# Optimization experiments

Hardware: AMD Instinct MI355X
Metric: run time of the kernel (lower is better)

The kernel has to match this reference:

```python
import jax, jax.numpy as jnp
import numpy as np

N = 16384
D_IN = 512
HEADS = 2
D_HEAD = 256
EPS_LN = 1e-5
NEG_SLOPE = 0.2


def l2norm_dim0(x):
    # F.normalize(x, p=2, dim=0): per-column L2 normalization
    n = jnp.sqrt(jnp.sum(x * x, axis=0, keepdims=True))
    return x / jnp.maximum(n, 1e-12)


def layer_norm(x, g, b):
    m = jnp.mean(x, axis=-1, keepdims=True)
    v = jnp.mean((x - m) ** 2, axis=-1, keepdims=True)
    return (x - m) * jax.lax.rsqrt(v + EPS_LN) * g + b


def gat_conv(x, edge_index, W, att_src, att_dst, bias):
    # PyG GATConv with add_self_loops=True, concat=True, negative_slope=0.2
    n = x.shape[0]
    loops = jnp.arange(n, dtype=edge_index.dtype)
    src = jnp.concatenate([edge_index[0], loops])
    dst = jnp.concatenate([edge_index[1], loops])
    h = (x @ W).reshape(n, HEADS, D_HEAD)            # [N, H, Dh]
    a_src = jnp.sum(h * att_src, axis=-1)            # [N, H]
    a_dst = jnp.sum(h * att_dst, axis=-1)            # [N, H]
    e = a_src[src] + a_dst[dst]                      # [E, H]
    e = jnp.where(e >= 0, e, NEG_SLOPE * e)          # leaky_relu
    # segment softmax over incoming edges of each dst node
    emax = jax.ops.segment_max(e, dst, num_segments=n)
    ex = jnp.exp(e - emax[dst])
    den = jax.ops.segment_sum(ex, dst, num_segments=n)
    alpha = ex / den[dst]                            # [E, H]
    msg = h[src] * alpha[:, :, None]                 # [E, H, Dh]
    out = jax.ops.segment_sum(msg, dst, num_segments=n)  # [N, H, Dh]
    return out.reshape(n, HEADS * D_HEAD) + bias


def setup_inputs() -> dict:
    key = jax.random.key(0)
    ks = jax.random.split(key, 16)
    def glorot(k, shape):
        lim = np.sqrt(6.0 / (shape[0] + shape[-1]))
        return jax.random.uniform(k, shape, jnp.float32, -lim, lim)
    x = jax.random.normal(ks[0], (N, D_IN), jnp.float32)
    edge_index = jax.random.randint(ks[1], (2, 524288), 0, N, jnp.int64)
    return {
        "x": x,
        "edge_index": edge_index,
        "W": glorot(ks[2], (D_IN, HEADS * D_HEAD)),
        "att_src": glorot(ks[3], (HEADS, D_HEAD)),
        "att_dst": glorot(ks[4], (HEADS, D_HEAD)),
        "bias_conv": jnp.zeros((HEADS * D_HEAD,), jnp.float32),
        "Wa": glorot(ks[5], (512, 256)), "ba": jnp.zeros((256,), jnp.float32),
        "ga": jnp.ones((256,), jnp.float32), "bga": jnp.zeros((256,), jnp.float32),
        "W1": glorot(ks[6], (256, 128)), "b1": jnp.zeros((128,), jnp.float32),
        "g1": jnp.ones((128,), jnp.float32), "bg1": jnp.zeros((128,), jnp.float32),
        "W2": glorot(ks[7], (128, 64)), "b2": jnp.zeros((64,), jnp.float32),
        "g2": jnp.ones((64,), jnp.float32), "bg2": jnp.zeros((64,), jnp.float32),
        "W3": glorot(ks[8], (64, 3)), "b3": jnp.zeros((3,), jnp.float32),
    }


def reference(x, edge_index, W, att_src, att_dst, bias_conv,
              Wa, ba, ga, bga, W1, b1, g1, bg1,
              W2, b2, g2, bg2, W3, b3):
    h = l2norm_dim0(x)
    h = gat_conv(h, edge_index, W, att_src, att_dst, bias_conv)
    h = jax.nn.relu(h)
    h = l2norm_dim0(h)
    h = layer_norm(h @ Wa + ba, ga, bga)
    h = jax.nn.relu(h)
    h = l2norm_dim0(h)
    h = layer_norm(h @ W1 + b1, g1, bg1)
    h = jax.nn.relu(h)
    h = l2norm_dim0(h)
    h = layer_norm(h @ W2 + b2, g2, bg2)
    h = jax.nn.relu(h)
    h = l2norm_dim0(h)
    h = h @ W3 + b3                                  # [N, 3]
    # torch.cdist(h, h, p=2)
    sq = jnp.sum(h * h, axis=-1)
    d2 = sq[:, None] + sq[None, :] - 2.0 * (h @ h.T)
    return jnp.sqrt(jnp.maximum(d2, 0.0))
```

## Files before the change

### kernel.cpp

```cpp
#include <hip/hip_runtime.h>
#include <math.h>


typedef __bf16 bf16x8 __attribute__((ext_vector_type(8)));
typedef __bf16 bf16x4 __attribute__((ext_vector_type(4)));
typedef __bf16 bf16x2 __attribute__((ext_vector_type(2)));
typedef float  f32x4  __attribute__((ext_vector_type(4)));
typedef short  short8 __attribute__((ext_vector_type(8)));

static __device__ __forceinline__ float leaky02(float e){ return e >= 0.f ? e : 0.2f*e; }

static __device__ __forceinline__ float wred_sum(float v){
  #pragma unroll
  for (int m = 1; m < 64; m <<= 1) v += __shfl_xor(v, m);
  return v;
}
static __device__ __forceinline__ float wred_max(float v){
  #pragma unroll
  for (int m = 1; m < 64; m <<= 1) v = fmaxf(v, __shfl_xor(v, m));
  return v;
}

__global__ void colnorm_sq(const float* __restrict__ X, float* __restrict__ ss, int R, int C){
  int c = blockIdx.x*blockDim.x + threadIdx.x;
  if (c >= C) return;
  int r0 = blockIdx.y * 128;
  int r1 = r0 + 128; if (r1 > R) r1 = R;
  float s = 0.f;
  for (int r = r0; r < r1; ++r){ float v = X[(size_t)r*C + c]; s = fmaf(v, v, s); }
  atomicAdd(&ss[c], s);
}

__global__ void scale_rows(const float* __restrict__ W, const float* __restrict__ ss,
                           float* __restrict__ Wo, int K, int C){
  int i = blockIdx.x*blockDim.x + threadIdx.x;
  if (i >= K*C) return;
  int row = i / C;
  float n = fmaxf(sqrtf(ss[row]), 1e-12f);
  Wo[i] = W[i] / n;
}

__global__ __launch_bounds__(256) void split_hl(const float* __restrict__ X,
    __bf16* __restrict__ H, __bf16* __restrict__ L, int n4){
  int i = blockIdx.x*256 + threadIdx.x;
  if (i >= n4) return;
  float4 v = ((const float4*)X)[i];
  bf16x4 hv, lv;
  hv[0] = (__bf16)v.x; lv[0] = (__bf16)(v.x - (float)hv[0]);
  hv[1] = (__bf16)v.y; lv[1] = (__bf16)(v.y - (float)hv[1]);
  hv[2] = (__bf16)v.z; lv[2] = (__bf16)(v.z - (float)hv[2]);
  hv[3] = (__bf16)v.w; lv[3] = (__bf16)(v.w - (float)hv[3]);
  ((bf16x4*)H)[i] = hv;
  ((bf16x4*)L)[i] = lv;
}

__global__ __launch_bounds__(256) void split_tr_scaled(const float* __restrict__ B,
    const float* __restrict__ ss,
    __bf16* __restrict__ TH, __bf16* __restrict__ TL, int K, int N){
  __shared__ float tile[32][33];
  int lx = threadIdx.x & 31, ly = threadIdx.x >> 5;
  int kb = blockIdx.y*32, nb = blockIdx.x*32;
  #pragma unroll
  for (int i = 0; i < 4; i++){
    int kr = kb + ly + i*8;
    float inv = 1.f / fmaxf(sqrtf(ss[kr]), 1e-12f);
    tile[ly + i*8][lx] = B[(size_t)kr*N + nb + lx] * inv;
  }
  __syncthreads();
  #pragma unroll
  for (int i = 0; i < 4; i++){
    int nl = ly + i*8;
    float v = tile[lx][nl];
    __bf16 h = (__bf16)v;
    TH[(size_t)(nb + nl)*K + kb + lx] = h;
    TL[(size_t)(nb + nl)*K + kb + lx] = (__bf16)(v - (float)h);
  }
}

__global__ __launch_bounds__(256) void gemm_bf16x3(
    const __bf16* __restrict__ Ah, const __bf16* __restrict__ Al,
    const __bf16* __restrict__ Bth, const __bf16* __restrict__ Btl,
    float* __restrict__ C, int M, int N, int K)
{
  __shared__ __align__(16) __bf16 sAh[128][40];
  __shared__ __align__(16) __bf16 sAl[128][40];
  __shared__ __align__(16) __bf16 sBh[64][40];
  __shared__ __align__(16) __bf16 sBl[64][40];
  int tid = threadIdx.x;
  int lane = tid & 63, wave = tid >> 6;
  int wr = wave >> 1, wc = wave & 1;
  int rowBase = blockIdx.x << 7, colBase = blockIdx.y << 6;

  int ar = tid >> 2;
  int ac = tid & 3;

  short8 rAh0, rAh1, rAl0, rAl1, rBh, rBl;
  auto loadA = [&](int k0){
    rAh0 = *(const short8*)(Ah + (size_t)(rowBase + ar     )*K + k0 + ac*8);
    rAh1 = *(const short8*)(Ah + (size_t)(rowBase + ar + 64)*K + k0 + ac*8);
    rAl0 = *(const short8*)(Al + (size_t)(rowBase + ar     )*K + k0 + ac*8);
    rAl1 = *(const short8*)(Al + (size_t)(rowBase + ar + 64)*K + k0 + ac*8);
    rBh  = *(const short8*)(Bth + (size_t)(colBase + ar)*K + k0 + ac*8);
    rBl  = *(const short8*)(Btl + (size_t)(colBase + ar)*K + k0 + ac*8);
  };

  f32x4 acc[4][2];
  #pragma unroll
  for (int m = 0; m < 4; m++)
    #pragma unroll
    for (int n = 0; n < 2; n++) acc[m][n] = (f32x4){0.f,0.f,0.f,0.f};

  loadA(0);
  int nsteps = K >> 5;
  for (int s = 0; s < nsteps; ++s){
    __syncthreads();
    *(short8*)&sAh[ar][ac*8]      = rAh0;
    *(short8*)&sAh[ar+64][ac*8]   = rAh1;
    *(short8*)&sAl[ar][ac*8]      = rAl0;
    *(short8*)&sAl[ar+64][ac*8]   = rAl1;
    *(short8*)&sBh[ar][ac*8]      = rBh;
    *(short8*)&sBl[ar][ac*8]      = rBl;
    if (s + 1 < nsteps) loadA((s+1) << 5);
    __syncthreads();

    int kslot = lane >> 4;
    bf16x8 fah[4], fal[4], fbh[2], fbl[2];
    #pragma unroll
    for (int m = 0; m < 4; m++){
      int r = wr*64 + m*16 + (lane & 15);
      fah[m] = *(const bf16x8*)&sAh[r][kslot*8];
      fal[m] = *(const bf16x8*)&sAl[r][kslot*8];
    }
    #pragma unroll
    for (int n = 0; n < 2; n++){
      int c = wc*32 + n*16 + (lane & 15);
      fbh[n] = *(const bf16x8*)&sBh[c][kslot*8];
      fbl[n] = *(const bf16x8*)&sBl[c][kslot*8];
    }
    #pragma unroll
    for (int m = 0; m < 4; m++)
      #pragma unroll
      for (int n = 0; n < 2; n++){
        acc[m][n] = __builtin_amdgcn_mfma_f32_16x16x32_bf16(fah[m], fbh[n], acc[m][n], 0,0,0);
        acc[m][n] = __builtin_amdgcn_mfma_f32_16x16x32_bf16(fah[m], fbl[n], acc[m][n], 0,0,0);
        acc[m][n] = __builtin_amdgcn_mfma_f32_16x16x32_bf16(fal[m], fbh[n], acc[m][n], 0,0,0);
      }
  }

  int rg = lane >> 4, cl = lane & 15;
  #pragma unroll
  for (int m = 0; m < 4; m++)
    #pragma unroll
    for (int n = 0; n < 2; n++)
      #pragma unroll
      for (int j = 0; j < 4; j++)
        C[(size_t)(rowBase + wr*64 + m*16 + rg*4 + j)*N + colBase + wc*32 + n*16 + cl] = acc[m][n][j];
}

__global__ __launch_bounds__(256) void att_kernel(const float* __restrict__ h,
    const float* __restrict__ att_src, const float* __restrict__ att_dst,
    float* __restrict__ asrc, float* __restrict__ adst, int N){
  int lane = threadIdx.x & 63;
  int node = blockIdx.x*4 + (threadIdx.x >> 6);
  const float4* hp = (const float4*)(h + (size_t)node*512);
  float4 v0 = hp[lane], v1 = hp[64 + lane];
  float4 as0 = ((const float4*)att_src)[lane], as1 = ((const float4*)att_src)[64+lane];
  float4 ad0 = ((const float4*)att_dst)[lane], ad1 = ((const float4*)att_dst)[64+lane];
  float s0 = v0.x*as0.x + v0.y*as0.y + v0.z*as0.z + v0.w*as0.w;
  float s1 = v1.x*as1.x + v1.y*as1.y + v1.z*as1.z + v1.w*as1.w;
  float d0 = v0.x*ad0.x + v0.y*ad0.y + v0.z*ad0.z + v0.w*ad0.w;
  float d1 = v1.x*ad1.x + v1.y*ad1.y + v1.z*ad1.z + v1.w*ad1.w;
  s0 = wred_sum(s0); s1 = wred_sum(s1); d0 = wred_sum(d0); d1 = wred_sum(d1);
  if (lane == 0){
    asrc[2*node] = s0; asrc[2*node+1] = s1;
    adst[2*node] = d0; adst[2*node+1] = d1;
  }
}

__global__ void deg_count(const int* __restrict__ dst, int* deg, int E){
  int e = blockIdx.x*blockDim.x + threadIdx.x;
  if (e < E) atomicAdd(&deg[dst[e]], 1);
}
__global__ __launch_bounds__(1024) void scan_kernel(const int* __restrict__ deg,
    int* __restrict__ offs, int* __restrict__ cursor, int n){
  __shared__ int part[1024];
  int t = threadIdx.x;
  int chunk = (n + 1023) >> 10;
  int base = t * chunk;
  int loc[32];
  int local = 0;
  for (int k = 0; k < chunk; k++){
    int idx = base + k; loc[k] = local;
    if (idx < n) local += deg[idx] + 1;
  }
  part[t] = local; __syncthreads();
  for (int off = 1; off < 1024; off <<= 1){
    int v = (t >= off) ? part[t-off] : 0; __syncthreads();
    part[t] += v; __syncthreads();
  }
  int excl = part[t] - local;
  for (int k = 0; k < chunk; k++){
    int idx = base + k;
    if (idx < n){ int o = excl + loc[k]; offs[idx] = o; cursor[idx] = o; }
  }
  if (t == 1023) offs[n] = part[1023];
}
__global__ void scatter_edges(const int* __restrict__ src, const int* __restrict__ dst,
                              int* cursor, int* __restrict__ ssrc, int E, int N){
  int e = blockIdx.x*blockDim.x + threadIdx.x;
  if (e < E){
    int d = dst[e]; int pos = atomicAdd(&cursor[d], 1); ssrc[pos] = src[e];
  } else if (e < E + N){
    int i = e - E; int pos = atomicAdd(&cursor[i], 1); ssrc[pos] = i;
  }
}

__global__ __launch_bounds__(256) void gat_aggregate(const float* __restrict__ h,
    const int* __restrict__ offs, const int* __restrict__ ssrc,
    const float* __restrict__ asrc, const float* __restrict__ adst,
    const float* __restrict__ bias, float* __restrict__ out,
    __bf16* __restrict__ H, __bf16* __restrict__ L, int N){
  __shared__ float cw[2][4];
  __shared__ int sidx[256];
  __shared__ float salpha[512];
  int d = blockIdx.x, t = threadIdx.x, lane = t & 63, wid = t >> 6;
  int beg = offs[d], end = offs[d+1], cnt = end - beg;
  float ad0 = adst[2*d], ad1 = adst[2*d+1];
  int dim = 2*t, head = t >> 7;
  float accx = 0.f, accy = 0.f;

  if (cnt <= 256){
    float le0 = -1e30f, le1 = -1e30f;
    if (t < cnt){
      int s = ssrc[beg + t]; sidx[t] = s;
      float2 a = *(const float2*)&asrc[2*s];
      le0 = leaky02(a.x + ad0); le1 = leaky02(a.y + ad1);
    }
    float m0 = wred_max(le0), m1 = wred_max(le1);
    if (lane == 0){ cw[0][wid] = m0; cw[1][wid] = m1; }
    __syncthreads();
    m0 = fmaxf(fmaxf(cw[0][0],cw[0][1]), fmaxf(cw[0][2],cw[0][3]));
    m1 = fmaxf(fmaxf(cw[1][0],cw[1][1]), fmaxf(cw[1][2],cw[1][3]));
    __syncthreads();
    float e0 = (t < cnt) ? __expf(le0 - m0) : 0.f;
    float e1 = (t < cnt) ? __expf(le1 - m1) : 0.f;
    float q0 = wred_sum(e0), q1 = wred_sum(e1);
    if (lane == 0){ cw[0][wid] = q0; cw[1][wid] = q1; }
    __syncthreads();
    float inv0 = 1.f / (cw[0][0]+cw[0][1]+cw[0][2]+cw[0][3]);
    float inv1 = 1.f / (cw[1][0]+cw[1][1]+cw[1][2]+cw[1][3]);
    if (t < cnt){ salpha[2*t] = e0*inv0; salpha[2*t+1] = e1*inv1; }
    __syncthreads();
    #pragma unroll 2
    for (int o = 0; o < cnt; ++o){
      int s = sidx[o];
      float al = salpha[2*o + head];
      float2 v = *(const float2*)&h[(size_t)s*512 + dim];
      accx = fmaf(al, v.x, accx); accy = fmaf(al, v.y, accy);
    }
  } else {
    float m0 = -1e30f, m1 = -1e30f;
    for (int o = beg + t; o < end; o += 256){
      int s = ssrc[o]; float2 a = *(const float2*)&asrc[2*s];
      m0 = fmaxf(m0, leaky02(a.x + ad0)); m1 = fmaxf(m1, leaky02(a.y + ad1));
    }
    m0 = wred_max(m0); m1 = wred_max(m1);
    if (lane == 0){ cw[0][wid] = m0; cw[1][wid] = m1; }
    __syncthreads();
    m0 = fmaxf(fmaxf(cw[0][0],cw[0][1]), fmaxf(cw[0][2],cw[0][3]));
    m1 = fmaxf(fmaxf(cw[1][0],cw[1][1]), fmaxf(cw[1][2],cw[1][3]));
    __syncthreads();
    float q0 = 0.f, q1 = 0.f;
    for (int o = beg + t; o < end; o += 256){
      int s = ssrc[o]; float2 a = *(const float2*)&asrc[2*s];
      q0 += __expf(leaky02(a.x + ad0) - m0); q1 += __expf(leaky02(a.y + ad1) - m1);
    }
    q0 = wred_sum(q0); q1 = wred_sum(q1);
    if (lane == 0){ cw[0][wid] = q0; cw[1][wid] = q1; }
    __syncthreads();
    float inv0 = 1.f / (cw[0][0]+cw[0][1]+cw[0][2]+cw[0][3]);
    float inv1 = 1.f / (cw[1][0]+cw[1][1]+cw[1][2]+cw[1][3]);
    __syncthreads();
    for (int c0 = beg; c0 < end; c0 += 256){
      int cc = end - c0; if (cc > 256) cc = 256;
      if (t < cc){
        int s = ssrc[c0 + t]; sidx[t] = s;
        float2 a = *(const float2*)&asrc[2*s];
        salpha[2*t]   = __expf(leaky02(a.x + ad0) - m0) * inv0;
        salpha[2*t+1] = __expf(leaky02(a.y + ad1) - m1) * inv1;
      }
      __syncthreads();
      for (int o = 0; o < cc; ++o){
        int s = sidx[o];
        float al = salpha[2*o + head];
        float2 v = *(const float2*)&h[(size_t)s*512 + dim];
        accx = fmaf(al, v.x, accx); accy = fmaf(al, v.y, accy);
      }
      __syncthreads();
    }
  }
  float ox = fmaxf(accx + bias[dim],   0.f);
  float oy = fmaxf(accy + bias[dim+1], 0.f);
  *(float2*)&out[(size_t)d*512 + dim] = make_float2(ox, oy);
  bf16x2 hv, lv;
  hv[0] = (__bf16)ox; lv[0] = (__bf16)(ox - (float)hv[0]);
  hv[1] = (__bf16)oy; lv[1] = (__bf16)(oy - (float)hv[1]);
  *(bf16x2*)&H[(size_t)d*512 + dim] = hv;
  *(bf16x2*)&L[(size_t)d*512 + dim] = lv;
}

template<int C, bool SPLIT>
__global__ __launch_bounds__(256) void ln_relu_t(float* __restrict__ Z,
    const float* __restrict__ bias, const float* __restrict__ g,
    const float* __restrict__ bg, __bf16* __restrict__ H, __bf16* __restrict__ L, int R){
  constexpr int VW = C / 64;
  int lane = threadIdx.x & 63, wid = threadIdx.x >> 6;
  int r = blockIdx.x*4 + wid;
  size_t base = (size_t)r*C + lane*VW;
  float v[VW], bi[VW], gm[VW], bt[VW];
  if constexpr (VW == 4){
    float4 t0 = *(const float4*)&Z[base];
    float4 t1 = *(const float4*)&bias[lane*4];
    float4 t2 = *(const float4*)&g[lane*4];
    float4 t3 = *(const float4*)&bg[lane*4];
    v[0]=t0.x; v[1]=t0.y; v[2]=t0.z; v[3]=t0.w;
    bi[0]=t1.x; bi[1]=t1.y; bi[2]=t1.z; bi[3]=t1.w;
    gm[0]=t2.x; gm[1]=t2.y; gm[2]=t2.z; gm[3]=t2.w;
    bt[0]=t3.x; bt[1]=t3.y; bt[2]=t3.z; bt[3]=t3.w;
  } else if constexpr (VW == 2){
    float2 t0 = *(const float2*)&Z[base];
    float2 t1 = *(const float2*)&bias[lane*2];
    float2 t2 = *(const float2*)&g[lane*2];
    float2 t3 = *(const float2*)&bg[lane*2];
    v[0]=t0.x; v[1]=t0.y; bi[0]=t1.x; bi[1]=t1.y;
    gm[0]=t2.x; gm[1]=t2.y; bt[0]=t3.x; bt[1]=t3.y;
  } else {
    v[0] = Z[base]; bi[0] = bias[lane]; gm[0] = g[lane]; bt[0] = bg[lane];
  }
  float sum = 0.f;
  #pragma unroll
  for (int j = 0; j < VW; j++){ v[j] += bi[j]; sum += v[j]; }
  sum = wred_sum(sum);
  float mean = sum * (1.f/C);
  float sq = 0.f;
  #pragma unroll
  for (int j = 0; j < VW; j++){ float dz = v[j]-mean; sq += dz*dz; }
  sq = wred_sum(sq);
  float rs = 1.f / sqrtf(sq*(1.f/C) + 1e-5f);
  float o[VW];
  #pragma unroll
  for (int j = 0; j < VW; j++) o[j] = fmaxf((v[j]-mean)*rs*gm[j] + bt[j], 0.f);
  if constexpr (VW == 4) *(float4*)&Z[base] = make_float4(o[0],o[1],o[2],o[3]);
  else if constexpr (VW == 2) *(float2*)&Z[base] = make_float2(o[0],o[1]);
  else Z[base] = o[0];
  if constexpr (SPLIT){
    if constexpr (VW == 4){
      bf16x4 hv, lv;
      #pragma unroll
      for (int j = 0; j < 4; j++){ hv[j] = (__bf16)o[j]; lv[j] = (__bf16)(o[j]-(float)hv[j]); }
      *(bf16x4*)&H[base] = hv; *(bf16x4*)&L[base] = lv;
    } else if constexpr (VW == 2){
      bf16x2 hv, lv;
      #pragma unroll
      for (int j = 0; j < 2; j++){ hv[j] = (__bf16)o[j]; lv[j] = (__bf16)(o[j]-(float)hv[j]); }
      *(bf16x2*)&H[base] = hv; *(bf16x2*)&L[base] = lv;
    } else {
      __bf16 hv = (__bf16)o[0];
      H[base] = hv; L[base] = (__bf16)(o[0]-(float)hv);
    }
  }
}

__global__ __launch_bounds__(256) void final_hf4(const float* __restrict__ A,
    const float* __restrict__ W3s, const float* __restrict__ b3,
    float4* __restrict__ hf4, int N){
  __shared__ float w[64*3];
  __shared__ float b[3];
  if (threadIdx.x < 192) w[threadIdx.x] = W3s[threadIdx.x];
  if (threadIdx.x < 3)   b[threadIdx.x] = b3[threadIdx.x];
  __syncthreads();
  int r = blockIdx.x*blockDim.x + threadIdx.x;
  if (r >= N) return;
  float x = b[0], y = b[1], z = b[2];
  #pragma unroll 8
  for (int k = 0; k < 64; ++k){
    float a = A[(size_t)r*64 + k];
    x = fmaf(a, w[k*3],   x);
    y = fmaf(a, w[k*3+1], y);
    z = fmaf(a, w[k*3+2], z);
  }
  float sq = x*x + y*y + z*z;
  hf4[r] = make_float4(x, y, z, sq);
}

__global__ __launch_bounds__(256) void cdist_kernel(const float4* __restrict__ hf,
                                                    float* __restrict__ out, int N){
  int i = blockIdx.y;
  int j0 = (blockIdx.x*256 + threadIdx.x)*4;
  float4 a = hf[i];
  float4 b0 = hf[j0], b1 = hf[j0+1], b2 = hf[j0+2], b3 = hf[j0+3];
  f32x4 r; float d;
  d = a.w + b0.w - 2.f*(a.x*b0.x + a.y*b0.y + a.z*b0.z); r[0] = sqrtf(fmaxf(d, 0.f));
  d = a.w + b1.w - 2.f*(a.x*b1.x + a.y*b1.y + a.z*b1.z); r[1] = sqrtf(fmaxf(d, 0.f));
  d = a.w + b2.w - 2.f*(a.x*b2.x + a.y*b2.y + a.z*b2.z); r[2] = sqrtf(fmaxf(d, 0.f));
  d = a.w + b3.w - 2.f*(a.x*b3.x + a.y*b3.y + a.z*b3.z); r[3] = sqrtf(fmaxf(d, 0.f));
  __builtin_nontemporal_store(r, (f32x4*)&out[(size_t)i*N + j0]);
}

extern "C" void kernel_launch(void* const* d_in, const int* in_sizes, int n_in,
                              void* d_out, int out_size, void* d_ws, size_t ws_size,
                              hipStream_t stream){
  const int N = in_sizes[0] / 512;
  const int E = in_sizes[1] / 2;

  const float* x         = (const float*)d_in[0];
  const int*   ei        = (const int*)  d_in[1];
  const float* W         = (const float*)d_in[2];
  const float* att_src   = (const float*)d_in[3];
  const float* att_dst   = (const float*)d_in[4];
  const float* bias_conv = (const float*)d_in[5];
  const float* Wa  = (const float*)d_in[6];
  const float* ba  = (const float*)d_in[7];
  const float* ga  = (const float*)d_in[8];
  const float* bga = (const float*)d_in[9];
  const float* W1  = (const float*)d_in[10];
  const float* b1  = (const float*)d_in[11];
  const float* g1  = (const float*)d_in[12];
  const float* bg1 = (const float*)d_in[13];
  const float* W2  = (const float*)d_in[14];
  const float* b2  = (const float*)d_in[15];
  const float* g2  = (const float*)d_in[16];
  const float* bg2 = (const float*)d_in[17];
  const float* W3  = (const float*)d_in[18];
  const float* b3  = (const float*)d_in[19];

  const int* e_src = ei;
  const int* e_dst = ei + E;

  size_t off = 0;
  auto alloc = [&](size_t bytes)->char*{
    size_t o = off; off += (bytes + 255) & ~(size_t)255;
    return (char*)d_ws + o;
  };
  float* bufA  = (float*)alloc((size_t)N*512*4);
  float* bufB  = (float*)alloc((size_t)N*512*4);
  __bf16* Ah   = (__bf16*)alloc((size_t)N*512*2);
  __bf16* Al   = (__bf16*)alloc((size_t)N*512*2);
  __bf16* Bth  = (__bf16*)alloc(512*512*2);
  __bf16* Btl  = (__bf16*)alloc(512*512*2);
  float* W3sc  = (float*)alloc(64*3*4);
  char* zbase  = alloc(5*512*4 + (size_t)N*4);
  float* ss1 = (float*)zbase;
  float* ss2 = ss1 + 512;
  float* ss3 = ss2 + 512;
  float* ss4 = ss3 + 512;
  float* ss5 = ss4 + 512;
  int*   deg = (int*)(ss5 + 512);
  float* asrc  = (float*)alloc((size_t)N*2*4);
  float* adst  = (float*)alloc((size_t)N*2*4);
  float4* hf4  = (float4*)alloc((size_t)N*16);
  int* offs    = (int*)alloc((size_t)(N+1)*4);
  int* cursor  = (int*)alloc((size_t)N*4);
  int* ssrc    = (int*)alloc((size_t)(E+N)*4);

  float* outF = (float*)d_out;

  hipMemsetAsync(zbase, 0, 5*512*4 + (size_t)N*4, stream);

  colnorm_sq<<<dim3(2,128), 256, 0, stream>>>(x, ss1, N, 512);
  split_hl<<<(N*512/4+255)/256, 256, 0, stream>>>(x, Ah, Al, N*512/4);
  split_tr_scaled<<<dim3(16,16), 256, 0, stream>>>(W, ss1, Bth, Btl, 512, 512);
  gemm_bf16x3<<<dim3(N/128, 8), 256, 0, stream>>>(Ah, Al, Bth, Btl, bufA, N, 512, 512);

  att_kernel<<<N/4, 256, 0, stream>>>(bufA, att_src, att_dst, asrc, adst, N);
  deg_count<<<(E+255)/256, 256, 0, stream>>>(e_dst, deg, E);
  scan_kernel<<<1, 1024, 0, stream>>>(deg, offs, cursor, N);
  scatter_edges<<<(E+N+255)/256, 256, 0, stream>>>(e_src, e_dst, cursor, ssrc, E, N);
  gat_aggregate<<<N, 256, 0, stream>>>(bufA, offs, ssrc, asrc, adst, bias_conv,
                                       bufB, Ah, Al, N);

  colnorm_sq<<<dim3(2,128), 256, 0, stream>>>(bufB, ss2, N, 512);
  split_tr_scaled<<<dim3(8,16), 256, 0, stream>>>(Wa, ss2, Bth, Btl, 512, 256);
  gemm_bf16x3<<<dim3(N/128, 4), 256, 0, stream>>>(Ah, Al, Bth, Btl, bufA, N, 256, 512);
  ln_relu_t<256,true><<<N/4, 256, 0, stream>>>(bufA, ba, ga, bga, Ah, Al, N);

  colnorm_sq<<<dim3(1,128), 256, 0, stream>>>(bufA, ss3, N, 256);
  split_tr_scaled<<<dim3(4,8), 256, 0, stream>>>(W1, ss3, Bth, Btl, 256, 128);
  gemm_bf16x3<<<dim3(N/128, 2), 256, 0, stream>>>(Ah, Al, Bth, Btl, bufB, N, 128, 256);
  ln_relu_t<128,true><<<N/4, 256, 0, stream>>>(bufB, b1, g1, bg1, Ah, Al, N);

  colnorm_sq<<<dim3(1,128), 256, 0, stream>>>(bufB, ss4, N, 128);
  split_tr_scaled<<<dim3(2,4), 256, 0, stream>>>(W2, ss4, Bth, Btl, 128, 64);
  gemm_bf16x3<<<dim3(N/128, 1), 256, 0, stream>>>(Ah, Al, Bth, Btl, bufA, N, 64, 128);
  ln_relu_t<64,false><<<N/4, 256, 0, stream>>>(bufA, b2, g2, bg2, (__bf16*)nullptr, (__bf16*)nullptr, N);

  colnorm_sq<<<dim3(1,128), 256, 0, stream>>>(bufA, ss5, N, 64);
  scale_rows<<<1, 256, 0, stream>>>(W3, ss5, W3sc, 64, 3);
  final_hf4<<<(N+255)/256, 256, 0, stream>>>(bufA, W3sc, b3, hf4, N);
  cdist_kernel<<<dim3(N/1024, N), 256, 0, stream>>>(hf4, outF, N);
}
```

Measured before the change: 765.1 us.

## Fuse input split into GEMM, wave-per-node GAT aggregation, drop fp32 GAT output

The first GEMM now reads fp32 x directly and splits it into bf16 hi/lo while staging to shared memory, which removes the separate split_hl pass over the input. GAT aggregation moves from one 256-thread block per node to one wave per node. Indices and attention weights are passed by shuffles instead of shared memory and barriers, and each lane loads 8 floats per neighbour. The fp32 GAT output write is removed, and its column norms are computed from the hi+lo bf16 pair. The W3 scaling is folded into final_hf4. The risk is more latency per wave on high-degree nodes and slightly different rounding in the norm.

Result: no change. 761.7 us (-0.4%).

```diff
diff --git a/kernel.cpp b/kernel.cpp
--- a/kernel.cpp
+++ b/kernel.cpp
@@ -31,27 +31,18 @@
   atomicAdd(&ss[c], s);
 }
 
-__global__ void scale_rows(const float* __restrict__ W, const float* __restrict__ ss,
-                           float* __restrict__ Wo, int K, int C){
-  int i = blockIdx.x*blockDim.x + threadIdx.x;
-  if (i >= K*C) return;
-  int row = i / C;
-  float n = fmaxf(sqrtf(ss[row]), 1e-12f);
-  Wo[i] = W[i] / n;
-}
-
-__global__ __launch_bounds__(256) void split_hl(const float* __restrict__ X,
-    __bf16* __restrict__ H, __bf16* __restrict__ L, int n4){
-  int i = blockIdx.x*256 + threadIdx.x;
-  if (i >= n4) return;
-  float4 v = ((const float4*)X)[i];
-  bf16x4 hv, lv;
-  hv[0] = (__bf16)v.x; lv[0] = (__bf16)(v.x - (float)hv[0]);
-  hv[1] = (__bf16)v.y; lv[1] = (__bf16)(v.y - (float)hv[1]);
-  hv[2] = (__bf16)v.z; lv[2] = (__bf16)(v.z - (float)hv[2]);
-  hv[3] = (__bf16)v.w; lv[3] = (__bf16)(v.w - (float)hv[3]);
-  ((bf16x4*)H)[i] = hv;
-  ((bf16x4*)L)[i] = lv;
+__global__ void colnorm_sq_hl(const __bf16* __restrict__ H, const __bf16* __restrict__ L,
+                              float* __restrict__ ss, int R, int C){
+  int c = blockIdx.x*blockDim.x + threadIdx.x;
+  if (c >= C) return;
+  int r0 = blockIdx.y * 128;
+  int r1 = r0 + 128; if (r1 > R) r1 = R;
+  float s = 0.f;
+  for (int r = r0; r < r1; ++r){
+    float v = (float)H[(size_t)r*C + c] + (float)L[(size_t)r*C + c];
+    s = fmaf(v, v, s);
+  }
+  atomicAdd(&ss[c], s);
 }
 
 __global__ __launch_bounds__(256) void split_tr_scaled(const float* __restrict__ B,
@@ -120,6 +111,93 @@
     *(short8*)&sAl[ar+64][ac*8]   = rAl1;
     *(short8*)&sBh[ar][ac*8]      = rBh;
     *(short8*)&sBl[ar][ac*8]      = rBl;
+    if (s + 1 < nsteps) loadA((s+1) << 5);
+    __syncthreads();
+
+    int kslot = lane >> 4;
+    bf16x8 fah[4], fal[4], fbh[2], fbl[2];
+    #pragma unroll
+    for (int m = 0; m < 4; m++){
+      int r = wr*64 + m*16 + (lane & 15);
+      fah[m] = *(const bf16x8*)&sAh[r][kslot*8];
+      fal[m] = *(const bf16x8*)&sAl[r][kslot*8];
+    }
+    #pragma unroll
+    for (int n = 0; n < 2; n++){
+      int c = wc*32 + n*16 + (lane & 15);
+      fbh[n] = *(const bf16x8*)&sBh[c][kslot*8];
+      fbl[n] = *(const bf16x8*)&sBl[c][kslot*8];
+    }
+    #pragma unroll
+    for (int m = 0; m < 4; m++)
+      #pragma unroll
+      for (int n = 0; n < 2; n++){
+        acc[m][n] = __builtin_amdgcn_mfma_f32_16x16x32_bf16(fah[m], fbh[n], acc[m][n], 0,0,0);
+        acc[m][n] = __builtin_amdgcn_mfma_f32_16x16x32_bf16(fah[m], fbl[n], acc[m][n], 0,0,0);
+        acc[m][n] = __builtin_amdgcn_mfma_f32_16x16x32_bf16(fal[m], fbh[n], acc[m][n], 0,0,0);
+      }
+  }
+
+  int rg = lane >> 4, cl = lane & 15;
+  #pragma unroll
+  for (int m = 0; m < 4; m++)
+    #pragma unroll
+    for (int n = 0; n < 2; n++)
+      #pragma unroll
+      for (int j = 0; j < 4; j++)
+        C[(size_t)(rowBase + wr*64 + m*16 + rg*4 + j)*N + colBase + wc*32 + n*16 + cl] = acc[m][n][j];
+}
+
+__global__ __launch_bounds__(256) void gemm_f32a_bf16x3(
+    const float* __restrict__ A,
+    const __bf16* __restrict__ Bth, const __bf16* __restrict__ Btl,
+    float* __restrict__ C, int M, int N, int K)
+{
+  __shared__ __align__(16) __bf16 sAh[128][40];
+  __shared__ __align__(16) __bf16 sAl[128][40];
+  __shared__ __align__(16) __bf16 sBh[64][40];
+  __shared__ __align__(16) __bf16 sBl[64][40];
+  int tid = threadIdx.x;
+  int lane = tid & 63, wave = tid >> 6;
+  int wr = wave >> 1, wc = wave & 1;
+  int rowBase = blockIdx.x << 7, colBase = blockIdx.y << 6;
+
+  int ar = tid >> 2;
+  int ac = tid & 3;
+
+  float4 rA0a, rA0b, rA1a, rA1b; short8 rBh, rBl;
+  auto loadA = [&](int k0){
+    const float* p0 = A + (size_t)(rowBase + ar)*K + k0 + ac*8;
+    rA0a = *(const float4*)p0; rA0b = *(const float4*)(p0 + 4);
+    const float* p1 = A + (size_t)(rowBase + ar + 64)*K + k0 + ac*8;
+    rA1a = *(const float4*)p1; rA1b = *(const float4*)(p1 + 4);
+    rBh  = *(const short8*)(Bth + (size_t)(colBase + ar)*K + k0 + ac*8);
+    rBl  = *(const short8*)(Btl + (size_t)(colBase + ar)*K + k0 + ac*8);
+  };
+  auto splitst = [&](float4 a, float4 b, __bf16* dh, __bf16* dl){
+    float t[8] = {a.x,a.y,a.z,a.w,b.x,b.y,b.z,b.w};
+    bf16x8 hv, lv;
+    #pragma unroll
+    for (int j = 0; j < 8; j++){
+      __bf16 h = (__bf16)t[j]; hv[j] = h; lv[j] = (__bf16)(t[j] - (float)h);
+    }
+    *(bf16x8*)dh = hv; *(bf16x8*)dl = lv;
+  };
+
+  f32x4 acc[4][2];
+  #pragma unroll
+  for (int m = 0; m < 4; m++)
+    #pragma unroll
+    for (int n = 0; n < 2; n++) acc[m][n] = (f32x4){0.f,0.f,0.f,0.f};
+
+  loadA(0);
+  int nsteps = K >> 5;
+  for (int s = 0; s < nsteps; ++s){
+    __syncthreads();
+    splitst(rA0a, rA0b, &sAh[ar][ac*8],    &sAl[ar][ac*8]);
+    splitst(rA1a, rA1b, &sAh[ar+64][ac*8], &sAl[ar+64][ac*8]);
+    *(short8*)&sBh[ar][ac*8] = rBh;
+    *(short8*)&sBl[ar][ac*8] = rBl;
     if (s + 1 < nsteps) loadA((s+1) << 5);
     __syncthreads();
 
@@ -215,98 +293,93 @@
   }
 }
 
-__global__ __launch_bounds__(256) void gat_aggregate(const float* __restrict__ h,
+__global__ __launch_bounds__(256) void gat_aggregate_w(const float* __restrict__ h,
     const int* __restrict__ offs, const int* __restrict__ ssrc,
     const float* __restrict__ asrc, const float* __restrict__ adst,
-    const float* __restrict__ bias, float* __restrict__ out,
+    const float* __restrict__ bias,
     __bf16* __restrict__ H, __bf16* __restrict__ L, int N){
-  __shared__ float cw[2][4];
-  __shared__ int sidx[256];
-  __shared__ float salpha[512];
-  int d = blockIdx.x, t = threadIdx.x, lane = t & 63, wid = t >> 6;
+  int lane = threadIdx.x & 63;
+  int d = blockIdx.x*4 + (threadIdx.x >> 6);
   int beg = offs[d], end = offs[d+1], cnt = end - beg;
   float ad0 = adst[2*d], ad1 = adst[2*d+1];
-  int dim = 2*t, head = t >> 7;
-  float accx = 0.f, accy = 0.f;
-
-  if (cnt <= 256){
-    float le0 = -1e30f, le1 = -1e30f;
-    if (t < cnt){
-      int s = ssrc[beg + t]; sidx[t] = s;
-      float2 a = *(const float2*)&asrc[2*s];
+
+  int dbase = lane*8;
+  bool head0 = dbase < 256;
+  f32x4 acc0 = {0.f,0.f,0.f,0.f}, acc1 = {0.f,0.f,0.f,0.f};
+
+  if (cnt <= 64){
+    int sreg = 0; float le0 = -1e30f, le1 = -1e30f;
+    if (lane < cnt){
+      sreg = ssrc[beg + lane];
+      float2 a = *(const float2*)&asrc[2*sreg];
       le0 = leaky02(a.x + ad0); le1 = leaky02(a.y + ad1);
     }
     float m0 = wred_max(le0), m1 = wred_max(le1);
-    if (lane == 0){ cw[0][wid] = m0; cw[1][wid] = m1; }
-    __syncthreads();
-    m0 = fmaxf(fmaxf(cw[0][0],cw[0][1]), fmaxf(cw[0][2],cw[0][3]));
-    m1 = fmaxf(fmaxf(cw[1][0],cw[1][1]), fmaxf(cw[1][2],cw[1][3]));
-    __syncthreads();
-    float e0 = (t < cnt) ? __expf(le0 - m0) : 0.f;
-    float e1 = (t < cnt) ? __expf(le1 - m1) : 0.f;
-    float q0 = wred_sum(e0), q1 = wred_sum(e1);
-    if (lane == 0){ cw[0][wid] = q0; cw[1][wid] = q1; }
-    __syncthreads();
-    float inv0 = 1.f / (cw[0][0]+cw[0][1]+cw[0][2]+cw[0][3]);
-    float inv1 = 1.f / (cw[1][0]+cw[1][1]+cw[1][2]+cw[1][3]);
-    if (t < cnt){ salpha[2*t] = e0*inv0; salpha[2*t+1] = e1*inv1; }
-    __syncthreads();
-    #pragma unroll 2
+    float e0 = (lane < cnt) ? __expf(le0 - m0) : 0.f;
+    float e1 = (lane < cnt) ? __expf(le1 - m1) : 0.f;
+    float inv0 = 1.f / wred_sum(e0), inv1 = 1.f / wred_sum(e1);
+    float al0 = e0*inv0, al1 = e1*inv1;
     for (int o = 0; o < cnt; ++o){
-      int s = sidx[o];
-      float al = salpha[2*o + head];
-      float2 v = *(const float2*)&h[(size_t)s*512 + dim];
-      accx = fmaf(al, v.x, accx); accy = fmaf(al, v.y, accy);
+      int s = __shfl(sreg, o);
+      float aA = __shfl(al0, o), aB = __shfl(al1, o);
+      float al = head0 ? aA : aB;
+      const float4* hp = (const float4*)&h[(size_t)s*512 + dbase];
+      float4 v0 = hp[0], v1 = hp[1];
+      acc0[0] = fmaf(al, v0.x, acc0[0]); acc0[1] = fmaf(al, v0.y, acc0[1]);
+      acc0[2] = fmaf(al, v0.z, acc0[2]); acc0[3] = fmaf(al, v0.w, acc0[3]);
+      acc1[0] = fmaf(al, v1.x, acc1[0]); acc1[1] = fmaf(al, v1.y, acc1[1]);
+      acc1[2] = fmaf(al, v1.z, acc1[2]); acc1[3] = fmaf(al, v1.w, acc1[3]);
     }
   } else {
     float m0 = -1e30f, m1 = -1e30f;
-    for (int o = beg + t; o < end; o += 256){
+    for (int o = beg + lane; o < end; o += 64){
       int s = ssrc[o]; float2 a = *(const float2*)&asrc[2*s];
       m0 = fmaxf(m0, leaky02(a.x + ad0)); m1 = fmaxf(m1, leaky02(a.y + ad1));
     }
     m0 = wred_max(m0); m1 = wred_max(m1);
-    if (lane == 0){ cw[0][wid] = m0; cw[1][wid] = m1; }
-    __syncthreads();
-    m0 = fmaxf(fmaxf(cw[0][0],cw[0][1]), fmaxf(cw[0][2],cw[0][3]));
-    m1 = fmaxf(fmaxf(cw[1][0],cw[1][1]), fmaxf(cw[1][2],cw[1][3]));
-    __syncthreads();
     float q0 = 0.f, q1 = 0.f;
-    for (int o = beg + t; o < end; o += 256){
+    for (int o = beg + lane; o < end; o += 64){
       int s = ssrc[o]; float2 a = *(const float2*)&asrc[2*s];
       q0 += __expf(leaky02(a.x + ad0) - m0); q1 += __expf(leaky02(a.y + ad1) - m1);
     }
-    q0 = wred_sum(q0); q1 = wred_sum(q1);
-    if (lane == 0){ cw[0][wid] = q0; cw[1][wid] = q1; }
-    __syncthreads();
-    float inv0 = 1.f / (cw[0][0]+cw[0][1]+cw[0][2]+cw[0][3]);
-    float inv1 = 1.f / (cw[1][0]+cw[1][1]+cw[1][2]+cw[1][3]);
-    __syncthreads();
-    for (int c0 = beg; c0 < end; c0 += 256){
-      int cc = end - c0; if (cc > 256) cc = 256;
-      if (t < cc){
-        int s = ssrc[c0 + t]; sidx[t] = s;
-        float2 a = *(const float2*)&asrc[2*s];
-        salpha[2*t]   = __expf(leaky02(a.x + ad0) - m0) * inv0;
-        salpha[2*t+1] = __expf(leaky02(a.y + ad1) - m1) * inv1;
+    float inv0 = 1.f / wred_sum(q0), inv1 = 1.f / wred_sum(q1);
+    for (int c0 = beg; c0 < end; c0 += 64){
+      int cc = end - c0; if (cc > 64) cc = 64;
+      int sreg = 0; float al0 = 0.f, al1 = 0.f;
+      if (lane < cc){
+        sreg = ssrc[c0 + lane];
+        float2 a = *(const float2*)&asrc[2*sreg];
+        al0 = __expf(leaky02(a.x + ad0) - m0) * inv0;
+        al1 = __expf(leaky02(a.y + ad1) - m1) * inv1;
       }
-      __syncthreads();
       for (int o = 0; o < cc; ++o){
-        int s = sidx[o];
-        float al = salpha[2*o + head];
-        float2 v = *(const float2*)&h[(size_t)s*512 + dim];
-        accx = fmaf(al, v.x, accx); accy = fmaf(al, v.y, accy);
+        int s = __shfl(sreg, o);
+        float aA = __shfl(al0, o), aB = __shfl(al1, o);
+        float al = head0 ? aA : aB;
+        const float4* hp = (const float4*)&h[(size_t)s*512 + dbase];
+        float4 v0 = hp[0], v1 = hp[1];
+        acc0[0] = fmaf(al, v0.x, acc0[0]); acc0[1] = fmaf(al, v0.y, acc0[1]);
+        acc0[2] = fmaf(al, v0.z, acc0[2]); acc0[3] = fmaf(al, v0.w, acc0[3]);
+        acc1[0] = fmaf(al, v1.x, acc1[0]); acc1[1] = fmaf(al, v1.y, acc1[1]);
+        acc1[2] = fmaf(al, v1.z, acc1[2]); acc1[3] = fmaf(al, v1.w, acc1[3]);
       }
-      __syncthreads();
-    }
-  }
-  float ox = fmaxf(accx + bias[dim],   0.f);
-  float oy = fmaxf(accy + bias[dim+1], 0.f);
-  *(float2*)&out[(size_t)d*512 + dim] = make_float2(ox, oy);
-  bf16x2 hv, lv;
-  hv[0] = (__bf16)ox; lv[0] = (__bf16)(ox - (float)hv[0]);
-  hv[1] = (__bf16)oy; lv[1] = (__bf16)(oy - (float)hv[1]);
-  *(bf16x2*)&H[(size_t)d*512 + dim] = hv;
-  *(bf16x2*)&L[(size_t)d*512 + dim] = lv;
+    }
+  }
+
+  float4 bi0 = *(const float4*)&bias[dbase];
+  float4 bi1 = *(const float4*)&bias[dbase + 4];
+  float o_[8];
+  o_[0] = fmaxf(acc0[0] + bi0.x, 0.f); o_[1] = fmaxf(acc0[1] + bi0.y, 0.f);
+  o_[2] = fmaxf(acc0[2] + bi0.z, 0.f); o_[3] = fmaxf(acc0[3] + bi0.w, 0.f);
+  o_[4] = fmaxf(acc1[0] + bi1.x, 0.f); o_[5] = fmaxf(acc1[1] + bi1.y, 0.f);
+  o_[6] = fmaxf(acc1[2] + bi1.z, 0.f); o_[7] = fmaxf(acc1[3] + bi1.w, 0.f);
+  bf16x8 hv, lv;
+  #pragma unroll
+  for (int j = 0; j < 8; j++){
+    __bf16 hh = (__bf16)o_[j]; hv[j] = hh; lv[j] = (__bf16)(o_[j] - (float)hh);
+  }
+  *(bf16x8*)&H[(size_t)d*512 + dbase] = hv;
+  *(bf16x8*)&L[(size_t)d*512 + dbase] = lv;
 }
 
 template<int C, bool SPLIT>
@@ -372,12 +445,15 @@
 }
 
 __global__ __launch_bounds__(256) void final_hf4(const float* __restrict__ A,
-    const float* __restrict__ W3s, const float* __restrict__ b3,
-    float4* __restrict__ hf4, int N){
+    const float* __restrict__ W3, const float* __restrict__ ss,
+    const float* __restrict__ b3, float4* __restrict__ hf4, int N){
   __shared__ float w[64*3];
   __shared__ float b[3];
-  if (threadIdx.x < 192) w[threadIdx.x] = W3s[threadIdx.x];
-  if (threadIdx.x < 3)   b[threadIdx.x] = b3[threadIdx.x];
+  if (threadIdx.x < 192){
+    int k = threadIdx.x / 3;
+    w[threadIdx.x] = W3[threadIdx.x] / fmaxf(sqrtf(ss[k]), 1e-12f);
+  }
+  if (threadIdx.x < 3) b[threadIdx.x] = b3[threadIdx.x];
   __syncthreads();
   int r = blockIdx.x*blockDim.x + threadIdx.x;
   if (r >= N) return;
@@ -448,7 +524,6 @@
   __bf16* Al   = (__bf16*)alloc((size_t)N*512*2);
   __bf16* Bth  = (__bf16*)alloc(512*512*2);
   __bf16* Btl  = (__bf16*)alloc(512*512*2);
-  float* W3sc  = (float*)alloc(64*3*4);
   char* zbase  = alloc(5*512*4 + (size_t)N*4);
   float* ss1 = (float*)zbase;
   float* ss2 = ss1 + 512;
@@ -468,34 +543,32 @@
   hipMemsetAsync(zbase, 0, 5*512*4 + (size_t)N*4, stream);
 
   colnorm_sq<<<dim3(2,128), 256, 0, stream>>>(x, ss1, N, 512);
-  split_hl<<<(N*512/4+255)/256, 256, 0, stream>>>(x, Ah, Al, N*512/4);
   split_tr_scaled<<<dim3(16,16), 256, 0, stream>>>(W, ss1, Bth, Btl, 512, 512);
-  gemm_bf16x3<<<dim3(N/128, 8), 256, 0, stream>>>(Ah, Al, Bth, Btl, bufA, N, 512, 512);
+  gemm_f32a_bf16x3<<<dim3(N/128, 8), 256, 0, stream>>>(x, Bth, Btl, bufA, N, 512, 512);
 
   att_kernel<<<N/4, 256, 0, stream>>>(bufA, att_src, att_dst, asrc, adst, N);
   deg_count<<<(E+255)/256, 256, 0, stream>>>(e_dst, deg, E);
   scan_kernel<<<1, 1024, 0, stream>>>(deg, offs, cursor, N);
   scatter_edges<<<(E+N+255)/256, 256, 0, stream>>>(e_src, e_dst, cursor, ssrc, E, N);
-  gat_aggregate<<<N, 256, 0, stream>>>(bufA, offs, ssrc, asrc, adst, bias_conv,
-                                       bufB, Ah, Al, N);
-
-  colnorm_sq<<<dim3(2,128), 256, 0, stream>>>(bufB, ss2, N, 512);
+  gat_aggregate_w<<<N/4, 256, 0, stream>>>(bufA, offs, ssrc, asrc, adst, bias_conv,
+                                           Ah, Al, N);
+
+  colnorm_sq_hl<<<dim3(2,128), 256, 0, stream>>>(Ah, Al, ss2, N, 512);
   split_tr_scaled<<<dim3(8,16), 256, 0, stream>>>(Wa, ss2, Bth, Btl, 512, 256);
-  gemm_bf16x3<<<dim3(N/128, 4), 256, 0, stream>>>(Ah, Al, Bth, Btl, bufA, N, 256, 512);
-  ln_relu_t<256,true><<<N/4, 256, 0, stream>>>(bufA, ba, ga, bga, Ah, Al, N);
-
-  colnorm_sq<<<dim3(1,128), 256, 0, stream>>>(bufA, ss3, N, 256);
+  gemm_bf16x3<<<dim3(N/128, 4), 256, 0, stream>>>(Ah, Al, Bth, Btl, bufB, N, 256, 512);
+  ln_relu_t<256,true><<<N/4, 256, 0, stream>>>(bufB, ba, ga, bga, Ah, Al, N);
+
+  colnorm_sq<<<dim3(1,128), 256, 0, stream>>>(bufB, ss3, N, 256);
   split_tr_scaled<<<dim3(4,8), 256, 0, stream>>>(W1, ss3, Bth, Btl, 256, 128);
-  gemm_bf16x3<<<dim3(N/128, 2), 256, 0, stream>>>(Ah, Al, Bth, Btl, bufB, N, 128, 256);
-  ln_relu_t<128,true><<<N/4, 256, 0, stream>>>(bufB, b1, g1, bg1, Ah, Al, N);
-
-  colnorm_sq<<<dim3(1,128), 256, 0, stream>>>(bufB, ss4, N, 128);
+  gemm_bf16x3<<<dim3(N/128, 2), 256, 0, stream>>>(Ah, Al, Bth, Btl, bufA, N, 128, 256);
+  ln_relu_t<128,true><<<N/4, 256, 0, stream>>>(bufA, b1, g1, bg1, Ah, Al, N);
+
+  colnorm_sq<<<dim3(1,128), 256, 0, stream>>>(bufA, ss4, N, 128);
   split_tr_scaled<<<dim3(2,4), 256, 0, stream>>>(W2, ss4, Bth, Btl, 128, 64);
-  gemm_bf16x3<<<dim3(N/128, 1), 256, 0, stream>>>(Ah, Al, Bth, Btl, bufA, N, 64, 128);
-  ln_relu_t<64,false><<<N/4, 256, 0, stream>>>(bufA, b2, g2, bg2, (__bf16*)nullptr, (__bf16*)nullptr, N);
-
-  colnorm_sq<<<dim3(1,128), 256, 0, stream>>>(bufA, ss5, N, 64);
-  scale_rows<<<1, 256, 0, stream>>>(W3, ss5, W3sc, 64, 3);
-  final_hf4<<<(N+255)/256, 256, 0, stream>>>(bufA, W3sc, b3, hf4, N);
+  gemm_bf16x3<<<dim3(N/128, 1), 256, 0, stream>>>(Ah, Al, Bth, Btl, bufB, N, 64, 128);
+  ln_relu_t<64,false><<<N/4, 256, 0, stream>>>(bufB, b2, g2, bg2, (__bf16*)nullptr, (__bf16*)nullptr, N);
+
+  colnorm_sq<<<dim3(1,128), 256, 0, stream>>>(bufB, ss5, N, 64);
+  final_hf4<<<(N+255)/256, 256, 0, stream>>>(bufB, W3, ss5, b3, hf4, N);
   cdist_kernel<<<dim3(N/1024, N), 256, 0, stream>>>(hf4, outF, N);
 }
```
